# Optimization experiments

Measured on AMD Instinct MI355X. Metric: run time of the kernel, lower is better.

The kernel has to match this reference:

```python
import jax, jax.numpy as jnp
import numpy as np

B, D, UNITS = 32768, 1024, 1024
NB_FACTOR, SPARSITY = 3, 32
NB = D // SPARSITY  # 32 blocks of 32x32 per block-diagonal factor


def _block_t_matmul(kb, y):
    # kb: [nb, bi, bo] block-diagonal factor values; y: [nb*bi, batch]
    # computes blockdiag(kb)^T @ y without materializing the dense matrix
    nb, bi, bo = kb.shape
    yb = y.reshape(nb, bi, -1)                      # [nb, bi, batch]
    out = jnp.einsum('nio,nib->nob', kb, yb)        # [nb, bo, batch]
    return out.reshape(nb * bo, -1)


def setup_inputs() -> dict:
    key = jax.random.key(0)
    ks = jax.random.split(key, 9)
    return {
        'x': jax.random.normal(ks[0], (B, D), jnp.float32),
        'P0': jax.random.normal(ks[1], (D, D), jnp.float32),
        'P1': jax.random.normal(ks[2], (D, D), jnp.float32),
        'P2': jax.random.normal(ks[3], (D, D), jnp.float32),
        'P3': jax.random.normal(ks[4], (UNITS, UNITS), jnp.float32),
        'K0': jax.random.normal(ks[5], (NB, SPARSITY, SPARSITY), jnp.float32) * 0.05,
        'K1': jax.random.normal(ks[6], (NB, SPARSITY, SPARSITY), jnp.float32) * 0.05,
        'K2': jax.random.normal(ks[7], (NB, SPARSITY, SPARSITY), jnp.float32) * 0.05,
        'bias': jax.random.normal(ks[8], (UNITS,), jnp.float32),
    }


def reference(x, P0, P1, P2, P3, K0, K1, K2, bias):
    # output = (softmax(P3) @ Bd2^T @ softmax(P2) @ Bd1^T @ softmax(P1) @ Bd0^T @ softmax(P0) @ x^T)^T + bias
    y = x.T                                          # [D, B]
    y = jax.nn.softmax(P0, axis=1) @ y
    for kb, perm in ((K0, P1), (K1, P2), (K2, P3)):
        y = _block_t_matmul(kb, y)
        y = jax.nn.softmax(perm, axis=1) @ y
    out = y.T + bias                                 # [B, UNITS]
    return out
```

## Files before the change

kernel.cpp:

```cpp
#include <hip/hip_runtime.h>
#include <hip/hip_bf16.h>

typedef __bf16 bf16x8 __attribute__((ext_vector_type(8)));
typedef float f32x4 __attribute__((ext_vector_type(4)));
typedef unsigned short u16x8 __attribute__((ext_vector_type(8)));

__device__ __forceinline__ unsigned short f2bf(float f) {
  unsigned u = __float_as_uint(f);
  u += 0x7FFF + ((u >> 16) & 1);
  return (unsigned short)(u >> 16);
}
__device__ __forceinline__ float bf2f(unsigned short h) {
  return __uint_as_float((unsigned)h << 16);
}

__device__ __forceinline__ void gload_lds16(const void* g, void* l) {
  __builtin_amdgcn_global_load_lds(
      (const __attribute__((address_space(1))) void*)g,
      (__attribute__((address_space(3))) void*)l, 16, 0, 0);
}

__device__ __forceinline__ void convert_slice(const float* __restrict__ x,
                                              unsigned short* __restrict__ xb,
                                              int base8, int cnt8, int cb, int nb)
{
  int i = cb * 256 + (int)threadIdx.x;
  const int stride = nb * 256;
  for (; i < cnt8; i += stride) {
    const size_t g = (size_t)(base8 + i);
    float4 v0 = ((const float4*)x)[2 * g];
    float4 v1 = ((const float4*)x)[2 * g + 1];
    u16x8 uv;
    uv[0] = f2bf(v0.x); uv[1] = f2bf(v0.y); uv[2] = f2bf(v0.z); uv[3] = f2bf(v0.w);
    uv[4] = f2bf(v1.x); uv[5] = f2bf(v1.y); uv[6] = f2bf(v1.z); uv[7] = f2bf(v1.w);
    ((u16x8*)xb)[g] = uv;
  }
}

__global__ __launch_bounds__(256)
void softmax4_kernel(const float* __restrict__ P0, const float* __restrict__ P1,
                     const float* __restrict__ P2, const float* __restrict__ P3,
                     unsigned short* __restrict__ S,
                     const float* __restrict__ cvx, unsigned short* __restrict__ cvxb,
                     int cvt_cnt)
{
  if (blockIdx.x >= 4096) {
    convert_slice(cvx, cvxb, 0, cvt_cnt, blockIdx.x - 4096, gridDim.x - 4096);
    return;
  }
  const int bid = blockIdx.x;
  const int mat = bid >> 10, row = bid & 1023;
  const float* P = (mat == 0 ? P0 : mat == 1 ? P1 : mat == 2 ? P2 : P3) + (size_t)row * 1024;
  unsigned short* out = S + ((size_t)mat << 20) + (size_t)row * 1024;
  const int t = threadIdx.x, w = t >> 6, l = t & 63;
  float4 v = ((const float4*)P)[t];
  float mx = fmaxf(fmaxf(v.x, v.y), fmaxf(v.z, v.w));
  #pragma unroll
  for (int off = 32; off > 0; off >>= 1) mx = fmaxf(mx, __shfl_xor(mx, off));
  __shared__ float redA[4], redB[4];
  if (l == 0) redA[w] = mx;
  __syncthreads();
  mx = fmaxf(fmaxf(redA[0], redA[1]), fmaxf(redA[2], redA[3]));
  float e0 = __expf(v.x - mx), e1 = __expf(v.y - mx);
  float e2 = __expf(v.z - mx), e3 = __expf(v.w - mx);
  float s = e0 + e1 + e2 + e3;
  #pragma unroll
  for (int off = 32; off > 0; off >>= 1) s += __shfl_xor(s, off);
  if (l == 0) redB[w] = s;
  __syncthreads();
  s = redB[0] + redB[1] + redB[2] + redB[3];
  float inv = 1.0f / s;
  ushort4 o;
  o.x = f2bf(e0 * inv); o.y = f2bf(e1 * inv);
  o.z = f2bf(e2 * inv); o.w = f2bf(e3 * inv);
  ((ushort4*)out)[t] = o;
}

__device__ __forceinline__ void bdT_body(const float* __restrict__ Kb,
                                         const unsigned short* __restrict__ in,
                                         unsigned short* __restrict__ outT, int bid)
{
  const int n = bid >> 2;
  const int c = (bid & 3) * 256 + threadIdx.x;
  __shared__ float Ks[32][33];
  for (int t = threadIdx.x; t < 1024; t += 256)
    Ks[t >> 5][t & 31] = Kb[n * 1024 + t];
  __syncthreads();
  float ri[32];
  #pragma unroll
  for (int i = 0; i < 32; ++i)
    ri[i] = bf2f(in[(size_t)(n * 32 + i) * 1024 + c]);
  unsigned short ov[32];
  #pragma unroll
  for (int o = 0; o < 32; ++o) {
    float acc = 0.f;
    #pragma unroll
    for (int i = 0; i < 32; ++i) acc = fmaf(Ks[i][o], ri[i], acc);
    ov[o] = f2bf(acc);
  }
  u16x8* dst = (u16x8*)(outT + (size_t)c * 1024 + n * 32);
  const u16x8* src = (const u16x8*)ov;
  #pragma unroll
  for (int q = 0; q < 4; ++q) dst[q] = src[q];
}

__global__ __launch_bounds__(256)
void blockdiagT_dual_kernel(const float* Ka, const unsigned short* ina, unsigned short* outa,
                            const float* Kb2, const unsigned short* inb, unsigned short* outb,
                            const float* cvx, unsigned short* cvxb, int cvt_base, int cvt_cnt)
{
  const int bid = blockIdx.x;
  if (bid >= 256) {
    convert_slice(cvx, cvxb, cvt_base, cvt_cnt, bid - 256, gridDim.x - 256);
    return;
  }
  const bool sec = bid >= 128;
  bdT_body(sec ? Kb2 : Ka, sec ? inb : ina, sec ? outb : outa, sec ? bid - 128 : bid);
}

template<int TILE, bool A_FP32, bool OUT_BIAS, bool RBD>
__device__ __forceinline__ void gemm_body(const void* __restrict__ Av,
                                          const unsigned short* __restrict__ B,
                                          void* __restrict__ Cv, const float* __restrict__ bias,
                                          int N, int K, int nprim, int bid,
                                          const float* __restrict__ KR)
{
  constexpr int FR  = TILE / 32;
  constexpr int SIT = TILE / 32;
  __shared__ unsigned short Asm[TILE * 64];
  __shared__ unsigned short Bsm[TILE * 64];
  const int tid = threadIdx.x;
  const int w = tid >> 6, l = tid & 63;
  const int cpx = nprim >> 3;
  const int swz = (bid & 7) * cpx + (bid >> 3);
  const int ntn = N / TILE;
  const int n0 = (swz % ntn) * TILE;
  const int m0 = (swz / ntn) * TILE;
  const int wr = (w >> 1) * (TILE / 2), wc = (w & 1) * (TILE / 2);
  const int lr = l & 15, kg = (l >> 4) << 3;

  f32x4 acc[FR][FR] = {};
  const int KT = K >> 6;
  for (int kt = 0; kt < KT; ++kt) {
    const int k0 = kt << 6;
    if (kt) __syncthreads();
    #pragma unroll
    for (int it = 0; it < SIT; ++it) {
      int li = it * 256 + tid;
      int row = li >> 3, c8 = (li & 7) << 3;
      const unsigned short* g = B + (size_t)(n0 + row) * K + (k0 + c8);
      gload_lds16(g, (char*)Bsm + it * 4096 + w * 1024);
    }
    if (A_FP32) {
      const float* Af = (const float*)Av;
      #pragma unroll
      for (int p = 0; p < SIT; ++p) {
        int row = (tid >> 3) + p * 32;
        int c8 = (tid & 7) << 3;
        const float* g = Af + (size_t)(m0 + row) * K + (k0 + c8);
        float4 v0 = ((const float4*)g)[0];
        float4 v1 = ((const float4*)g)[1];
        u16x8 uv;
        uv[0] = f2bf(v0.x); uv[1] = f2bf(v0.y); uv[2] = f2bf(v0.z); uv[3] = f2bf(v0.w);
        uv[4] = f2bf(v1.x); uv[5] = f2bf(v1.y); uv[6] = f2bf(v1.z); uv[7] = f2bf(v1.w);
        *(u16x8*)&Asm[row * 64 + c8] = uv;
      }
    } else {
      const unsigned short* Ab = (const unsigned short*)Av;
      #pragma unroll
      for (int it = 0; it < SIT; ++it) {
        int li = it * 256 + tid;
        int row = li >> 3, c8 = (li & 7) << 3;
        const unsigned short* g = Ab + (size_t)(m0 + row) * K + (k0 + c8);
        gload_lds16(g, (char*)Asm + it * 4096 + w * 1024);
      }
    }
    __syncthreads();
    #pragma unroll
    for (int ks = 0; ks < 2; ++ks) {
      const int kb = ks * 32 + kg;
      bf16x8 af[FR], bfr[FR];
      #pragma unroll
      for (int i = 0; i < FR; ++i)
        af[i] = *(const bf16x8*)&Asm[(wr + i * 16 + lr) * 64 + kb];
      #pragma unroll
      for (int j = 0; j < FR; ++j)
        bfr[j] = *(const bf16x8*)&Bsm[(wc + j * 16 + lr) * 64 + kb];
      #pragma unroll
      for (int i = 0; i < FR; ++i)
        #pragma unroll
        for (int j = 0; j < FR; ++j)
          acc[i][j] = __builtin_amdgcn_mfma_f32_16x16x32_bf16(af[i], bfr[j], acc[i][j], 0, 0, 0);
    }
  }
  const int cr = (l >> 4) << 2;
  const int cc = l & 15;
  if (RBD) {
    __shared__ float tileS[64][65];
    __shared__ float Kt[2][32][33];
    __syncthreads();
    #pragma unroll
    for (int j = 0; j < FR; ++j)
      #pragma unroll
      for (int i = 0; i < FR; ++i)
        #pragma unroll
        for (int r = 0; r < 4; ++r)
          tileS[wr + i * 16 + cr + r][wc + j * 16 + cc] = acc[i][j][r];
    for (int idx = tid; idx < 2048; idx += 256) {
      int blk = idx >> 10, rem = idx & 1023;
      Kt[blk][rem >> 5][rem & 31] = KR[(size_t)((n0 >> 5) + blk) * 1024 + rem];
    }
    __syncthreads();
    const int row = tid & 63, cq = (tid >> 6) << 4;
    const int nb2 = cq >> 5, co = cq & 31;
    float av[16] = {};
    #pragma unroll 4
    for (int o = 0; o < 32; ++o) {
      float a = tileS[row][nb2 * 32 + o];
      #pragma unroll
      for (int ii = 0; ii < 16; ++ii)
        av[ii] = fmaf(a, Kt[nb2][o][co + ii], av[ii]);
    }
    u16x8 ov[2];
    #pragma unroll
    for (int ii = 0; ii < 16; ++ii) ov[ii >> 3][ii & 7] = f2bf(av[ii]);
    unsigned short* Cz = (unsigned short*)Cv;
    u16x8* dst = (u16x8*)&Cz[(size_t)(m0 + row) * N + n0 + cq];
    dst[0] = ov[0]; dst[1] = ov[1];
  } else if (OUT_BIAS) {
    float* C = (float*)Cv;
    #pragma unroll
    for (int j = 0; j < FR; ++j) {
      int col = n0 + wc + j * 16 + cc;
      float bv = bias[col];
      #pragma unroll
      for (int i = 0; i < FR; ++i) {
        int rbase = m0 + wr + i * 16 + cr;
        #pragma unroll
        for (int r = 0; r < 4; ++r)
          C[(size_t)(rbase + r) * N + col] = acc[i][j][r] + bv;
      }
    }
  } else {
    unsigned short* C = (unsigned short*)Cv;
    #pragma unroll
    for (int j = 0; j < FR; ++j) {
      int col = n0 + wc + j * 16 + cc;
      #pragma unroll
      for (int i = 0; i < FR; ++i) {
        int rbase = m0 + wr + i * 16 + cr;
        #pragma unroll
        for (int r = 0; r < 4; ++r)
          C[(size_t)(rbase + r) * N + col] = f2bf(acc[i][j][r]);
      }
    }
  }
}

template<int TILE, bool A_FP32, bool OUT_BIAS>
__global__ __launch_bounds__(256)
void gemm_bt_kernel(const void* __restrict__ Av, const unsigned short* __restrict__ B,
                    void* __restrict__ Cv, const float* __restrict__ bias,
                    int N, int K, int nprim,
                    const float* cvx, unsigned short* cvxb, int cvt_base, int cvt_cnt)
{
  if ((int)blockIdx.x >= nprim) {
    convert_slice(cvx, cvxb, cvt_base, cvt_cnt, blockIdx.x - nprim, gridDim.x - nprim);
    return;
  }
  gemm_body<TILE, A_FP32, OUT_BIAS, false>(Av, B, Cv, bias, N, K, nprim, blockIdx.x, nullptr);
}

__global__ __launch_bounds__(256)
void gemm_dual_kernel(const unsigned short* A0, const unsigned short* B0, unsigned short* C0,
                      const unsigned short* A1, const unsigned short* B1, unsigned short* C1,
                      const float* KR,
                      const float* cvx, unsigned short* cvxb, int cvt_base, int cvt_cnt)
{
  const int bid = blockIdx.x;
  if (bid >= 512) {
    convert_slice(cvx, cvxb, cvt_base, cvt_cnt, bid - 512, gridDim.x - 512);
    return;
  }
  if (bid < 256)
    gemm_body<64, false, false, false>(A0, B0, (void*)C0, nullptr, 1024, 1024, 256, bid, nullptr);
  else
    gemm_body<64, false, false, true>(A1, B1, (void*)C1, nullptr, 1024, 1024, 256, bid - 256, KR);
}

__global__ __launch_bounds__(512, 2)
void gemm256_kernel(const unsigned short* __restrict__ A,
                    const unsigned short* __restrict__ B,
                    float* __restrict__ C, const float* __restrict__ bias,
                    int N, int K)
{
  extern __shared__ __align__(16) char lds[];
  const int tid = threadIdx.x;
  const int w = tid >> 6, l = tid & 63;
  const int wm = w >> 2, wn = w & 3;
  const int lr = l & 15;
  const int klo = (l >> 4) << 4;
  const int sw  = (lr & 7) << 4;

  const int nwg = gridDim.x;
  const int bid = blockIdx.x;
  const int cpx = nwg >> 3;
  const int swz = (bid & 7) * cpx + (bid >> 3);
  const int ntn = N >> 8;
  const int n0 = (swz % ntn) << 8;
  const int m0 = (swz / ntn) << 8;

  unsigned int aoff[2][2], boff[2][2];
  #pragma unroll
  for (int q = 0; q < 2; ++q)
    #pragma unroll
    for (int it = 0; it < 2; ++it) {
      int L = it * 8192 + tid * 16;
      int r = L >> 7;
      int cs = (L & 127) ^ ((r & 7) << 4);
      aoff[q][it] = (unsigned)(m0 + q * 128 + r) * K + (cs >> 1);
      boff[q][it] = (unsigned)(n0 + q * 128 + r) * K + (cs >> 1);
    }
  char* ldsA = lds;
  char* ldsB = lds + 65536;
  const int wdst = w * 1024;

#define STG_A(bufo, q, k0) do { \
    gload_lds16(A + aoff[q][0] + (k0), ldsA + (bufo) + (q) * 16384 + wdst); \
    gload_lds16(A + aoff[q][1] + (k0), ldsA + (bufo) + (q) * 16384 + 8192 + wdst); } while (0)
#define STG_B(bufo, q, k0) do { \
    gload_lds16(B + boff[q][0] + (k0), ldsB + (bufo) + (q) * 16384 + wdst); \
    gload_lds16(B + boff[q][1] + (k0), ldsB + (bufo) + (q) * 16384 + 8192 + wdst); } while (0)

  f32x4 acc[2][2][4][2] = {};

  STG_A(0, 0, 0); STG_B(0, 0, 0); STG_B(0, 1, 0); STG_A(0, 1, 0);

  const int NT = K >> 6;
  int curo = 0;
  for (int t = 0; t < NT; ++t) {
    const int nxto = curo ^ 32768;
    const int k1 = (t + 1) << 6;
    asm volatile("s_waitcnt vmcnt(0)" ::: "memory");
    __builtin_amdgcn_s_barrier();
    if (t + 1 < NT) { STG_A(nxto, 0, k1); STG_B(nxto, 0, k1); STG_B(nxto, 1, k1); STG_A(nxto, 1, k1); }
    const char* Ab = ldsA + curo;
    const char* Bb = ldsB + curo;
    bf16x8 av[2][2][4];
    bf16x8 bvr[2][2][2];
    #pragma unroll
    for (int ks = 0; ks < 2; ++ks) {
      const int cb = (ks * 64 + klo) ^ sw;
      #pragma unroll
      for (int qi = 0; qi < 2; ++qi)
        #pragma unroll
        for (int i = 0; i < 4; ++i)
          av[ks][qi][i] = *(const bf16x8*)(Ab + qi * 16384 + (wm * 64 + i * 16 + lr) * 128 + cb);
      #pragma unroll
      for (int qj = 0; qj < 2; ++qj)
        #pragma unroll
        for (int j = 0; j < 2; ++j)
          bvr[ks][qj][j] = *(const bf16x8*)(Bb + qj * 16384 + (wn * 32 + j * 16 + lr) * 128 + cb);
    }
    __builtin_amdgcn_s_setprio(1);
    #pragma unroll
    for (int ks = 0; ks < 2; ++ks)
      #pragma unroll
      for (int qi = 0; qi < 2; ++qi)
        #pragma unroll
        for (int i = 0; i < 4; ++i)
          #pragma unroll
          for (int qj = 0; qj < 2; ++qj)
            #pragma unroll
            for (int j = 0; j < 2; ++j)
              acc[qi][qj][i][j] = __builtin_amdgcn_mfma_f32_16x16x32_bf16(
                  av[ks][qi][i], bvr[ks][qj][j], acc[qi][qj][i][j], 0, 0, 0);
    __builtin_amdgcn_s_setprio(0);
    curo = nxto;
  }

  const int cr = (l >> 4) << 2;
  const int cc = l & 15;
  #pragma unroll
  for (int qi = 0; qi < 2; ++qi)
    #pragma unroll
    for (int qj = 0; qj < 2; ++qj)
      #pragma unroll
      for (int j = 0; j < 2; ++j) {
        const int col = n0 + qj * 128 + wn * 32 + j * 16 + cc;
        const float bvv = bias[col];
        #pragma unroll
        for (int i = 0; i < 4; ++i) {
          const int rbase = m0 + qi * 128 + wm * 64 + i * 16 + cr;
          #pragma unroll
          for (int r = 0; r < 4; ++r)
            C[(size_t)(rbase + r) * N + col] = acc[qi][qj][i][j][r] + bvv;
        }
      }
#undef STG_A
#undef STG_B
}

extern "C" void kernel_launch(void* const* d_in, const int* in_sizes, int n_in,
                              void* d_out, int out_size, void* d_ws, size_t ws_size,
                              hipStream_t stream) {
  (void)in_sizes; (void)n_in; (void)out_size;
  const float* x    = (const float*)d_in[0];
  const float* P0   = (const float*)d_in[1];
  const float* P1   = (const float*)d_in[2];
  const float* P2   = (const float*)d_in[3];
  const float* P3   = (const float*)d_in[4];
  const float* K0   = (const float*)d_in[5];
  const float* K1   = (const float*)d_in[6];
  const float* K2   = (const float*)d_in[7];
  const float* bias = (const float*)d_in[8];

  unsigned short* S  = (unsigned short*)d_ws;
  unsigned short* s0 = S;
  unsigned short* s1 = S + (1u << 20);
  unsigned short* s2 = S + (2u << 20);
  unsigned short* s3 = S + (3u << 20);
  unsigned short* t0 = S + (4u << 20);
  unsigned short* t1 = S + (5u << 20);
  unsigned short* Xb = S + (6u << 20);
  const size_t need = ((size_t)6 * (1u << 20) + (size_t)32768 * 1024) * 2;
  const bool have_xb = ws_size >= need;
  unsigned short* xbp = have_xb ? Xb : nullptr;

  const int SL = 524288;
  const int cvt3 = have_xb ? 3 * SL : 0;
  const int cvt1 = have_xb ? SL : 0;
  const int tail_big = have_xb ? 2048 : 0;
  const int tail_sm  = have_xb ? 512 : 0;

  softmax4_kernel<<<4096 + tail_big, 256, 0, stream>>>(P0, P1, P2, P3, S, x, xbp, cvt3);

  blockdiagT_dual_kernel<<<256 + tail_big, 256, 0, stream>>>(K2, s2, t0, K0, s0, t1,
                                                             x, xbp, 3 * SL, cvt3);

  gemm_dual_kernel<<<512 + tail_sm, 256, 0, stream>>>(s3, t0, s0, t1, s1, s2, K1,
                                                      x, xbp, 6 * SL, cvt1);

  gemm_bt_kernel<64, false, false><<<256 + tail_sm, 256, 0, stream>>>((const void*)s0, s2,
      (void*)t0, nullptr, 1024, 1024, 256, x, xbp, 7 * SL, cvt1);

  bool ok256 = false;
  if (have_xb) {
    hipError_t e = hipFuncSetAttribute((const void*)gemm256_kernel,
                                       hipFuncAttributeMaxDynamicSharedMemorySize, 131072);
    ok256 = (e == hipSuccess);
  }
  if (ok256) {
    gemm256_kernel<<<512, 512, 131072, stream>>>(Xb, t0, (float*)d_out, bias, 1024, 1024);
  } else if (have_xb) {
    gemm_bt_kernel<128, false, true><<<2048, 256, 0, stream>>>((const void*)Xb, t0,
        d_out, bias, 1024, 1024, 2048, nullptr, nullptr, 0, 0);
  } else {
    gemm_bt_kernel<128, true, true><<<2048, 256, 0, stream>>>((const void*)x, t0,
        d_out, bias, 1024, 1024, 2048, nullptr, nullptr, 0, 0);
  }
}
```

Baseline: 159.2 us.

## Split GEMM main loop into quadrant phases with finer-grained staged prefetch

Restructures the bf16 GEMM main loop into eight phases per two K-tiles. Each phase computes one 128x128 quadrant and issues the global-to-LDS loads for the next quadrant tiles, which lands later data in buffer regions the previous phase has finished with. Partial vmcnt waits and barriers around each phase replace the single wait-all-then-barrier per tile, so memory latency can overlap MFMA work more steadily. The cost is more barriers per tile and a more fragile buffer-reuse schedule that assumes K is a multiple of 128.

```diff
diff --git a/kernel.cpp b/kernel.cpp
--- a/kernel.cpp
+++ b/kernel.cpp
@@ -332,51 +332,57 @@
     gload_lds16(B + boff[q][0] + (k0), ldsB + (bufo) + (q) * 16384 + wdst); \
     gload_lds16(B + boff[q][1] + (k0), ldsB + (bufo) + (q) * 16384 + 8192 + wdst); } while (0)
 
+#define PH(BUFO, QI, QJ, STG, VM) do { \
+    bf16x8 a_[2][4], b_[2][2]; \
+    { const char* Ah = ldsA + (BUFO) + (QI) * 16384; \
+      const char* Bh = ldsB + (BUFO) + (QJ) * 16384; \
+      _Pragma("unroll") for (int ks = 0; ks < 2; ++ks) { \
+        const int cb = (ks * 64 + klo) ^ sw; \
+        _Pragma("unroll") for (int i = 0; i < 4; ++i) \
+          a_[ks][i] = *(const bf16x8*)(Ah + (wm * 64 + i * 16 + lr) * 128 + cb); \
+        _Pragma("unroll") for (int j = 0; j < 2; ++j) \
+          b_[ks][j] = *(const bf16x8*)(Bh + (wn * 32 + j * 16 + lr) * 128 + cb); } } \
+    STG; \
+    VM; \
+    __builtin_amdgcn_s_barrier(); \
+    asm volatile("s_waitcnt lgkmcnt(0)" ::: "memory"); \
+    __builtin_amdgcn_sched_barrier(0); \
+    __builtin_amdgcn_s_setprio(1); \
+    _Pragma("unroll") for (int ks = 0; ks < 2; ++ks) \
+      _Pragma("unroll") for (int i = 0; i < 4; ++i) \
+        _Pragma("unroll") for (int j = 0; j < 2; ++j) \
+          acc[QI][QJ][i][j] = __builtin_amdgcn_mfma_f32_16x16x32_bf16( \
+              a_[ks][i], b_[ks][j], acc[QI][QJ][i][j], 0, 0, 0); \
+    __builtin_amdgcn_s_setprio(0); \
+    __builtin_amdgcn_s_barrier(); \
+  } while (0)
+
+#define VM4 asm volatile("s_waitcnt vmcnt(4)" ::: "memory")
+#define VM0 asm volatile("s_waitcnt vmcnt(0)" ::: "memory")
+
   f32x4 acc[2][2][4][2] = {};
 
   STG_A(0, 0, 0); STG_B(0, 0, 0); STG_B(0, 1, 0); STG_A(0, 1, 0);
-
-  const int NT = K >> 6;
-  int curo = 0;
-  for (int t = 0; t < NT; ++t) {
-    const int nxto = curo ^ 32768;
-    const int k1 = (t + 1) << 6;
-    asm volatile("s_waitcnt vmcnt(0)" ::: "memory");
-    __builtin_amdgcn_s_barrier();
-    if (t + 1 < NT) { STG_A(nxto, 0, k1); STG_B(nxto, 0, k1); STG_B(nxto, 1, k1); STG_A(nxto, 1, k1); }
-    const char* Ab = ldsA + curo;
-    const char* Bb = ldsB + curo;
-    bf16x8 av[2][2][4];
-    bf16x8 bvr[2][2][2];
-    #pragma unroll
-    for (int ks = 0; ks < 2; ++ks) {
-      const int cb = (ks * 64 + klo) ^ sw;
-      #pragma unroll
-      for (int qi = 0; qi < 2; ++qi)
-        #pragma unroll
-        for (int i = 0; i < 4; ++i)
-          av[ks][qi][i] = *(const bf16x8*)(Ab + qi * 16384 + (wm * 64 + i * 16 + lr) * 128 + cb);
-      #pragma unroll
-      for (int qj = 0; qj < 2; ++qj)
-        #pragma unroll
-        for (int j = 0; j < 2; ++j)
-          bvr[ks][qj][j] = *(const bf16x8*)(Bb + qj * 16384 + (wn * 32 + j * 16 + lr) * 128 + cb);
-    }
-    __builtin_amdgcn_s_setprio(1);
-    #pragma unroll
-    for (int ks = 0; ks < 2; ++ks)
-      #pragma unroll
-      for (int qi = 0; qi < 2; ++qi)
-        #pragma unroll
-        for (int i = 0; i < 4; ++i)
-          #pragma unroll
-          for (int qj = 0; qj < 2; ++qj)
-            #pragma unroll
-            for (int j = 0; j < 2; ++j)
-              acc[qi][qj][i][j] = __builtin_amdgcn_mfma_f32_16x16x32_bf16(
-                  av[ks][qi][i], bvr[ks][qj][j], acc[qi][qj][i][j], 0, 0, 0);
-    __builtin_amdgcn_s_setprio(0);
-    curo = nxto;
+  STG_A(32768, 0, 64); STG_B(32768, 0, 64);
+  VM4;
+  __builtin_amdgcn_s_barrier();
+
+  const int NIT = K >> 7;
+  for (int it = 0; it < NIT; ++it) {
+    const int k1 = (2 * it + 1) << 6;
+    const int k2 = (2 * it + 2) << 6;
+    const int k3 = (2 * it + 3) << 6;
+    const bool s23 = (it < NIT - 1);
+    PH(0, 0, 0, { STG_B(32768, 1, k1); STG_A(32768, 1, k1); }, {});
+    PH(0, 0, 1, {}, {});
+    PH(0, 1, 0, { if (s23) STG_A(0, 0, k2); }, {});
+    PH(0, 1, 1, { if (s23) STG_B(0, 0, k2); },
+       { if (s23) { VM4; } else { VM0; } });
+    PH(32768, 0, 0, { if (s23) { STG_B(0, 1, k2); STG_A(0, 1, k2); } }, {});
+    PH(32768, 0, 1, {}, {});
+    PH(32768, 1, 0, { if (s23) STG_A(32768, 0, k3); }, {});
+    PH(32768, 1, 1, { if (s23) STG_B(32768, 0, k3); },
+       { if (s23) { VM4; } });
   }
 
   const int cr = (l >> 4) << 2;
@@ -399,6 +405,9 @@
       }
 #undef STG_A
 #undef STG_B
+#undef PH
+#undef VM4
+#undef VM0
 }
 
 extern "C" void kernel_launch(void* const* d_in, const int* in_sizes, int n_in,
```

Result: slower. 168.9 us (+6.1%).
